# Kernel tuning notes

Hardware: AMD Instinct MI355X
Metric: run time of the kernel (lower is better)

Reference implementation:

```python
import jax, jax.numpy as jnp
import numpy as np

B, L, K, D = 1024, 128, 16, 512
NUM_FEATURES, NUM_LABELS, NUM_NEG = 100000, 131072, 2048
EPS = 0.1
C = 2.0 + EPS  # spherical kernel constant


def safe_log(x, eps=1e-08):
    return jnp.log(jnp.maximum(x, eps))


def safe_normalize(x, axis=-1, eps=0.0001):
    norm = jnp.linalg.norm(x, axis=axis, keepdims=True)
    return x / jnp.maximum(norm, eps)


def setup_inputs() -> dict:
    key = jax.random.key(0)
    k0, k1, k2, k3, k4 = jax.random.split(key, 5)
    indices = jax.random.randint(k0, (B, L), 0, NUM_FEATURES)
    mask = jnp.ones((B, L), jnp.float32)
    labels = jax.random.randint(k1, (B, K), 0, NUM_LABELS)
    label_mask = jnp.ones((B, K), jnp.float32)
    neg_indices = jax.random.randint(k2, (NUM_NEG,), 0, NUM_LABELS)
    embed_table = jax.random.normal(k3, (NUM_FEATURES, D), jnp.float32) * 0.02
    W_kernel = jax.random.normal(k4, (D, NUM_LABELS), jnp.float32) * 0.02  # nnx.Linear kernel (in, out)
    return {"indices": indices, "mask": mask, "labels": labels,
            "label_mask": label_mask, "neg_indices": neg_indices,
            "embed_table": embed_table, "W_kernel": W_kernel}


def reference(indices, mask, labels, label_mask, neg_indices, embed_table, W_kernel):
    # MeanEmbedding encoder
    embeds = embed_table[indices]                                  # [B, L, D]
    sum_embeds = jnp.sum(embeds * mask[:, :, None], axis=1)        # [B, D]
    enc = sum_embeds / jnp.maximum(jnp.sum(mask, axis=1, keepdims=True), 1.0)
    query = safe_normalize(enc, axis=-1)                           # [B, D]
    W = safe_normalize(W_kernel.T, axis=-1)                        # [NUM_LABELS, D]

    safe_labels = jnp.maximum(labels, 0)
    all_indices = jnp.concatenate([safe_labels.reshape(-1), neg_indices])  # [B*K + NN]
    W_subset = W[all_indices]                                      # [B*K+NN, D]

    # spherical Yat kernel: dot^2 / max(C - 2*dot, eps)
    dot = jnp.clip(query @ W_subset.T, -0.999, 0.999)              # [B, B*K+NN]
    scores = dot ** 2 / jnp.maximum(C - 2.0 * dot, EPS)

    idx_offsets = jnp.arange(B)[:, None] * K + jnp.arange(K)[None, :]
    pos_scores = jnp.take_along_axis(scores, idx_offsets, axis=1)  # [B, K]
    neg_scores = scores[:, B * K:]                                 # [B, NN]
    all_scores = jnp.concatenate([pos_scores, neg_scores], axis=1) + 1e-08
    log_Z = jax.scipy.special.logsumexp(safe_log(all_scores), axis=1)
    log_probs = safe_log(pos_scores + 1e-08) - log_Z[:, None]
    return -jnp.sum(log_probs * label_mask) / (jnp.sum(label_mask) + 1e-06)
```

## Files before the change

### kernel.cpp

```cpp
#include <hip/hip_runtime.h>
#include <hip/hip_bf16.h>

#define BDIM 1024
#define LDIM 128
#define KDIM 16
#define DDIM 512
#define NFEAT 100000
#define NLAB 131072
#define NNEG 2048
#define NPOS (BDIM * KDIM)
#define NSUB (NPOS + NNEG)
#define EPSV 0.1f
#define CV 2.1f

typedef __attribute__((ext_vector_type(8))) short s8v;
typedef __attribute__((ext_vector_type(4))) float f4v;

static __device__ __forceinline__ unsigned short f2bf(float x) {
    union { float f; unsigned u; } v; v.f = x;
    unsigned r = v.u + 0x7FFF + ((v.u >> 16) & 1);
    return (unsigned short)(r >> 16);
}
static __device__ __forceinline__ float bf2f(unsigned short h) {
    return __uint_as_float((unsigned)h << 16);
}

__global__ __launch_bounds__(256) void init_kernel(int* __restrict__ cnt,
                                                   float* __restrict__ norms2,
                                                   float* __restrict__ Zrow,
                                                   float* __restrict__ accum) {
    int j = blockIdx.x * 256 + threadIdx.x;
    cnt[j] = 0;
    if (j < NSUB) norms2[j] = 0.f;
    if (j < BDIM) Zrow[j] = 0.f;
    if (j < 2) accum[j] = 0.f;
}

__global__ __launch_bounds__(256) void count_kernel(const int* __restrict__ labels,
                                                    const int* __restrict__ negs,
                                                    int* __restrict__ all_idx,
                                                    int* __restrict__ cnt) {
    int j = blockIdx.x * 256 + threadIdx.x;
    if (j >= NSUB) return;
    int v = (j < NPOS) ? max(labels[j], 0) : negs[j - NPOS];
    all_idx[j] = v;
    atomicAdd(&cnt[v], 1);
}

__global__ __launch_bounds__(256) void scan1_kernel(const int* __restrict__ cnt,
                                                    int* __restrict__ offs,
                                                    int* __restrict__ bsum) {
    int t = threadIdx.x;
    int base = blockIdx.x * 512;
    int a0 = cnt[base + 2 * t], a1 = cnt[base + 2 * t + 1];
    int chunk = a0 + a1;
    int ts = chunk;
    int lane = t & 63, wid = t >> 6;
    #pragma unroll
    for (int off = 1; off < 64; off <<= 1) {
        int v = __shfl_up(ts, off, 64);
        if (lane >= off) ts += v;
    }
    __shared__ int wsum[4];
    if (lane == 63) wsum[wid] = ts;
    __syncthreads();
    int woff = 0;
    for (int w = 0; w < wid; ++w) woff += wsum[w];
    int incl = woff + ts;
    int excl = incl - chunk;
    offs[base + 2 * t]     = excl;
    offs[base + 2 * t + 1] = excl + a0;
    if (t == 255) bsum[blockIdx.x] = incl;
}

__global__ __launch_bounds__(256) void scan2_kernel(const int* __restrict__ bsum,
                                                    int* __restrict__ bofs) {
    int t = threadIdx.x;
    int a = bsum[t];
    int ts = a;
    int lane = t & 63, wid = t >> 6;
    #pragma unroll
    for (int off = 1; off < 64; off <<= 1) {
        int v = __shfl_up(ts, off, 64);
        if (lane >= off) ts += v;
    }
    __shared__ int wsum[4];
    if (lane == 63) wsum[wid] = ts;
    __syncthreads();
    int woff = 0;
    for (int w = 0; w < wid; ++w) woff += wsum[w];
    bofs[t] = woff + ts - a;
}

__global__ __launch_bounds__(256) void scan3_kernel(int* __restrict__ offs,
                                                    const int* __restrict__ bofs) {
    int v = blockIdx.x * 256 + threadIdx.x;
    offs[v] += bofs[v >> 9];
}

__global__ __launch_bounds__(256) void place_kernel(const int* __restrict__ all_idx,
                                                    int* __restrict__ offs,
                                                    int* __restrict__ srt_v,
                                                    int* __restrict__ rank) {
    int j = blockIdx.x * 256 + threadIdx.x;
    if (j >= NSUB) return;
    int v = all_idx[j];
    int r = atomicAdd(&offs[v], 1);
    srt_v[r] = v;
    rank[j] = r;
}

__global__ __launch_bounds__(256) void query_kernel(const int* __restrict__ indices,
                                                    const float* __restrict__ mask,
                                                    const float* __restrict__ embed,
                                                    float* __restrict__ query,
                                                    unsigned short* __restrict__ qbf) {
    __shared__ int   sidx[LDIM];
    __shared__ float smask[LDIM];
    int b = blockIdx.x;
    int t = threadIdx.x;
    if (t < LDIM) {
        sidx[t]  = indices[b * LDIM + t];
        smask[t] = mask[b * LDIM + t];
    }
    __syncthreads();

    float ax = 0.f, ay = 0.f, msum = 0.f;
    #pragma unroll 2
    for (int l = 0; l < LDIM; l += 4) {
        int   i0 = sidx[l],     i1 = sidx[l + 1],  i2 = sidx[l + 2],  i3 = sidx[l + 3];
        float m0 = smask[l],    m1 = smask[l + 1], m2 = smask[l + 2], m3 = smask[l + 3];
        float2 r0 = *(const float2*)&embed[(size_t)i0 * DDIM + t * 2];
        float2 r1 = *(const float2*)&embed[(size_t)i1 * DDIM + t * 2];
        float2 r2 = *(const float2*)&embed[(size_t)i2 * DDIM + t * 2];
        float2 r3 = *(const float2*)&embed[(size_t)i3 * DDIM + t * 2];
        msum += m0 + m1 + m2 + m3;
        ax += m0 * r0.x + m1 * r1.x + m2 * r2.x + m3 * r3.x;
        ay += m0 * r0.y + m1 * r1.y + m2 * r2.y + m3 * r3.y;
    }
    float denom = fmaxf(msum, 1.0f);
    ax /= denom; ay /= denom;

    float ss = ax * ax + ay * ay;
    #pragma unroll
    for (int off = 32; off > 0; off >>= 1) ss += __shfl_down(ss, off, 64);
    __shared__ float red[4];
    __shared__ float snorm;
    int wid = t >> 6, lane = t & 63;
    if (lane == 0) red[wid] = ss;
    __syncthreads();
    if (t == 0) snorm = sqrtf(red[0] + red[1] + red[2] + red[3]);
    __syncthreads();
    float inv = 1.f / fmaxf(snorm, 1e-4f);
    float2 o = { ax * inv, ay * inv };
    *(float2*)&query[(size_t)b * DDIM + t * 2] = o;
    ushort2 ob = { f2bf(o.x), f2bf(o.y) };
    *(ushort2*)&qbf[(size_t)b * DDIM + t * 2] = ob;
}

__global__ __launch_bounds__(256) void gather_kernel(const float* __restrict__ Wk,
                                                     const int* __restrict__ srt_v,
                                                     unsigned short* __restrict__ Wsrt) {
    int d = blockIdx.x;
    int half = blockIdx.y;
    const float* row = Wk + (size_t)d * NLAB;
    unsigned short* o = Wsrt + (size_t)d * NSUB;
    int r0 = half * (NSUB / 2), r1 = r0 + NSUB / 2;
    #pragma unroll 4
    for (int r = r0 + threadIdx.x; r < r1; r += 256) {
        int v = srt_v[r];
        o[r] = f2bf(__builtin_nontemporal_load(&row[v]));
    }
}

__global__ __launch_bounds__(256) void transpose_kernel(const unsigned short* __restrict__ Wsrt,
                                                        unsigned short* __restrict__ WT,
                                                        float* __restrict__ norms2) {
    __shared__ unsigned short tile[64][66];
    __shared__ float psum[64];
    int t = threadIdx.x;
    int r0 = blockIdx.x * 64;
    int d0 = blockIdx.y * 64;
    if (t < 64) psum[t] = 0.f;
    __syncthreads();
    float local = 0.f;
    int rl = t & 63;
    #pragma unroll 4
    for (int it = 0; it < 16; ++it) {
        int dl = it * 4 + (t >> 6);
        unsigned short v = Wsrt[(size_t)(d0 + dl) * NSUB + r0 + rl];
        tile[rl][dl] = v;
        float f = bf2f(v);
        local += f * f;
    }
    atomicAdd(&psum[rl], local);
    __syncthreads();
    #pragma unroll 4
    for (int it = 0; it < 16; ++it) {
        int rr = it * 4 + (t >> 6);
        WT[(size_t)(r0 + rr) * DDIM + d0 + rl] = tile[rr][rl];
    }
    if (t < 64) atomicAdd(&norms2[r0 + t], psum[t]);
}

__global__ __launch_bounds__(256) void pos_kernel(const float* __restrict__ query,
                                                  const unsigned short* __restrict__ WT,
                                                  const int* __restrict__ rank,
                                                  const float* __restrict__ norms2,
                                                  float* __restrict__ pos_scores,
                                                  float* __restrict__ Zrow) {
    int t = threadIdx.x;
    int w = t >> 6, l = t & 63;
    int b = blockIdx.x * 4 + w;
    int j = b * KDIM + (l & 15);
    int r = rank[j];
    int g = l >> 4;
    const unsigned short* wrow = WT + (size_t)r * DDIM + g * 128;
    const float* qrow = query + (size_t)b * DDIM + g * 128;
    float acc = 0.f;
    #pragma unroll
    for (int kk = 0; kk < 128; kk += 8) {
        ushort4 w0 = *(const ushort4*)&wrow[kk];
        ushort4 w1 = *(const ushort4*)&wrow[kk + 4];
        float4 q0 = *(const float4*)&qrow[kk];
        float4 q1 = *(const float4*)&qrow[kk + 4];
        acc += bf2f(w0.x) * q0.x + bf2f(w0.y) * q0.y + bf2f(w0.z) * q0.z + bf2f(w0.w) * q0.w
             + bf2f(w1.x) * q1.x + bf2f(w1.y) * q1.y + bf2f(w1.z) * q1.z + bf2f(w1.w) * q1.w;
    }
    acc += __shfl_xor(acc, 16, 64);
    acc += __shfl_xor(acc, 32, 64);
    if (l < 16) {
        float nrm = fmaxf(sqrtf(norms2[r]), 1e-4f);
        float dot = fminf(fmaxf(acc / nrm, -0.999f), 0.999f);
        float sc = dot * dot / fmaxf(CV - 2.f * dot, EPSV);
        pos_scores[j] = sc;
        float s = sc;
        s += __shfl_xor(s, 1, 64); s += __shfl_xor(s, 2, 64);
        s += __shfl_xor(s, 4, 64); s += __shfl_xor(s, 8, 64);
        if (l == 0) atomicAdd(&Zrow[b], s);
    }
}

static __device__ __forceinline__ float score_of(float acc, float nn) {
    float dot = acc / nn;
    dot = fminf(fmaxf(dot, -0.999f), 0.999f);
    return dot * dot / fmaxf(CV - 2.f * dot, EPSV);
}

__global__ __launch_bounds__(256) void neg_kernel(const unsigned short* __restrict__ qbf,
                                                  const unsigned short* __restrict__ WT,
                                                  const int* __restrict__ rank,
                                                  const float* __restrict__ norms2,
                                                  float* __restrict__ Zrow) {
    __shared__ float rowsum[64];
    int t = threadIdx.x;
    int w = t >> 6, l = t & 63;
    int wm = w >> 1, wn = w & 1;
    int lr = l & 15, lg = l >> 4;
    int m0 = blockIdx.x * 64 + wm * 32;
    int n0 = blockIdx.y * 64 + wn * 32;
    if (t < 64) rowsum[t] = 0.f;
    __syncthreads();

    int rB0 = rank[NPOS + n0 + lr];
    int rB1 = rank[NPOS + n0 + 16 + lr];
    const unsigned short* a0p = qbf + (size_t)(m0 + lr) * DDIM + lg * 8;
    const unsigned short* a1p = qbf + (size_t)(m0 + 16 + lr) * DDIM + lg * 8;
    const unsigned short* b0p = WT + (size_t)rB0 * DDIM + lg * 8;
    const unsigned short* b1p = WT + (size_t)rB1 * DDIM + lg * 8;

    f4v acc00 = {0.f, 0.f, 0.f, 0.f}, acc01 = acc00, acc10 = acc00, acc11 = acc00;
    #pragma unroll
    for (int k0 = 0; k0 < DDIM; k0 += 32) {
        s8v a0 = *(const s8v*)(a0p + k0);
        s8v a1 = *(const s8v*)(a1p + k0);
        s8v b0 = *(const s8v*)(b0p + k0);
        s8v b1 = *(const s8v*)(b1p + k0);
        acc00 = __builtin_amdgcn_mfma_f32_16x16x32_bf16(a0, b0, acc00, 0, 0, 0);
        acc01 = __builtin_amdgcn_mfma_f32_16x16x32_bf16(a0, b1, acc01, 0, 0, 0);
        acc10 = __builtin_amdgcn_mfma_f32_16x16x32_bf16(a1, b0, acc10, 0, 0, 0);
        acc11 = __builtin_amdgcn_mfma_f32_16x16x32_bf16(a1, b1, acc11, 0, 0, 0);
    }

    float nn0 = fmaxf(sqrtf(norms2[rB0]), 1e-4f);
    float nn1 = fmaxf(sqrtf(norms2[rB1]), 1e-4f);
    float s[8];
    #pragma unroll
    for (int i = 0; i < 4; ++i) {
        s[i]     = score_of(acc00[i], nn0) + score_of(acc01[i], nn1);
        s[4 + i] = score_of(acc10[i], nn0) + score_of(acc11[i], nn1);
    }
    #pragma unroll
    for (int i = 0; i < 8; ++i) {
        s[i] += __shfl_xor(s[i], 1, 64);
        s[i] += __shfl_xor(s[i], 2, 64);
        s[i] += __shfl_xor(s[i], 4, 64);
        s[i] += __shfl_xor(s[i], 8, 64);
    }
    if (lr == 0) {
        #pragma unroll
        for (int i = 0; i < 4; ++i) {
            atomicAdd(&rowsum[wm * 32 + lg * 4 + i], s[i]);
            atomicAdd(&rowsum[wm * 32 + 16 + lg * 4 + i], s[4 + i]);
        }
    }
    __syncthreads();
    if (t < 64) atomicAdd(&Zrow[blockIdx.x * 64 + t], rowsum[t]);
}

__global__ __launch_bounds__(256) void finalize_kernel(const float* __restrict__ pos_scores,
                                                       const float* __restrict__ label_mask,
                                                       const float* __restrict__ Zrow,
                                                       float* __restrict__ accum) {
    int j = blockIdx.x * 256 + threadIdx.x;
    int b = j >> 4;
    float lm = label_mask[j];
    float logZ = logf(Zrow[b] + (float)(KDIM + NNEG) * 1e-8f);
    float v = lm * (logf(pos_scores[j] + 1e-8f) - logZ);
    #pragma unroll
    for (int off = 32; off > 0; off >>= 1) {
        v  += __shfl_down(v, off, 64);
        lm += __shfl_down(lm, off, 64);
    }
    __shared__ float rv[4], rl[4];
    int wid = threadIdx.x >> 6, lane = threadIdx.x & 63;
    if (lane == 0) { rv[wid] = v; rl[wid] = lm; }
    __syncthreads();
    if (threadIdx.x == 0) {
        atomicAdd(&accum[0], rv[0] + rv[1] + rv[2] + rv[3]);
        atomicAdd(&accum[1], rl[0] + rl[1] + rl[2] + rl[3]);
    }
}

__global__ void writeout_kernel(const float* __restrict__ accum, float* __restrict__ out) {
    out[0] = -accum[0] / (accum[1] + 1e-6f);
}

extern "C" void kernel_launch(void* const* d_in, const int* in_sizes, int n_in,
                              void* d_out, int out_size, void* d_ws, size_t ws_size,
                              hipStream_t stream) {
    const int*   indices    = (const int*)  d_in[0];
    const float* mask       = (const float*)d_in[1];
    const int*   labels     = (const int*)  d_in[2];
    const float* label_mask = (const float*)d_in[3];
    const int*   negs       = (const int*)  d_in[4];
    const float* embed      = (const float*)d_in[5];
    const float* Wk         = (const float*)d_in[6];
    float* out = (float*)d_out;

    unsigned short* Wsrt = (unsigned short*)d_ws;
    unsigned short* WT   = Wsrt + (size_t)DDIM * NSUB;
    float* query      = (float*)(WT + (size_t)NSUB * DDIM);
    unsigned short* qbf = (unsigned short*)(query + (size_t)BDIM * DDIM);
    int*   all_idx    = (int*)(qbf + (size_t)BDIM * DDIM);
    int*   srt_v      = all_idx + NSUB;
    int*   rank       = srt_v + NSUB;
    float* norms2     = (float*)(rank + NSUB);
    float* pos_scores = norms2 + NSUB;
    float* Zrow       = pos_scores + NPOS;
    float* accum      = Zrow + BDIM;
    int*   cnt        = (int*)(accum + 2);
    int*   offs       = cnt + NLAB;
    int*   bsum       = offs + NLAB;
    int*   bofs       = bsum + 256;

    init_kernel<<<NLAB / 256, 256, 0, stream>>>(cnt, norms2, Zrow, accum);
    count_kernel<<<NSUB / 256, 256, 0, stream>>>(labels, negs, all_idx, cnt);
    query_kernel<<<BDIM, 256, 0, stream>>>(indices, mask, embed, query, qbf);
    scan1_kernel<<<NLAB / 512, 256, 0, stream>>>(cnt, offs, bsum);
    scan2_kernel<<<1, 256, 0, stream>>>(bsum, bofs);
    scan3_kernel<<<NLAB / 256, 256, 0, stream>>>(offs, bofs);
    place_kernel<<<NSUB / 256, 256, 0, stream>>>(all_idx, offs, srt_v, rank);
    gather_kernel<<<dim3(DDIM, 2), 256, 0, stream>>>(Wk, srt_v, Wsrt);
    transpose_kernel<<<dim3(NSUB / 64, DDIM / 64), 256, 0, stream>>>(Wsrt, WT, norms2);
    pos_kernel<<<NPOS / 64, 256, 0, stream>>>(query, WT, rank, norms2, pos_scores, Zrow);
    neg_kernel<<<dim3(BDIM / 64, NNEG / 64), 256, 0, stream>>>(qbf, WT, rank, norms2, Zrow);
    finalize_kernel<<<NPOS / 256, 256, 0, stream>>>(pos_scores, label_mask, Zrow, accum);
    writeout_kernel<<<1, 1, 0, stream>>>(accum, out);
}
```

Before: 152.5 us.

## Coarsen label sort buckets, fuse gather with transpose, merge kernels and drop writeout

Label sorting now uses 512 coarse buckets keyed on the high bits of the index instead of a full 131072-entry counting sort. That removes the large init and the three-pass scan in favour of a single one-block scan. The W gather is fused into the transpose, so columns are read straight from W_kernel into the shared tile, and the intermediate Wsrt buffer plus one kernel launch go away. The query and gather-transpose kernels are merged into one launch, as are the pos and neg scoring kernels. The final writeout moves into finalize through a last-block ticket. This cuts launch count and intermediate memory traffic, but the gather reads within a 64-row tile are now strided and less coalesced.

```diff
diff --git a/kernel.cpp b/kernel.cpp
--- a/kernel.cpp
+++ b/kernel.cpp
@@ -5,13 +5,14 @@
 #define LDIM 128
 #define KDIM 16
 #define DDIM 512
-#define NFEAT 100000
 #define NLAB 131072
 #define NNEG 2048
 #define NPOS (BDIM * KDIM)
 #define NSUB (NPOS + NNEG)
 #define EPSV 0.1f
 #define CV 2.1f
+#define NBUCK 512
+#define GT_BLOCKS ((NSUB / 64) * (DDIM / 64))
 
 typedef __attribute__((ext_vector_type(8))) short s8v;
 typedef __attribute__((ext_vector_type(4))) float f4v;
@@ -28,12 +29,14 @@
 __global__ __launch_bounds__(256) void init_kernel(int* __restrict__ cnt,
                                                    float* __restrict__ norms2,
                                                    float* __restrict__ Zrow,
-                                                   float* __restrict__ accum) {
+                                                   float* __restrict__ accum,
+                                                   int* __restrict__ ticket) {
     int j = blockIdx.x * 256 + threadIdx.x;
-    cnt[j] = 0;
     if (j < NSUB) norms2[j] = 0.f;
+    if (j < NBUCK) cnt[j] = 0;
     if (j < BDIM) Zrow[j] = 0.f;
     if (j < 2) accum[j] = 0.f;
+    if (j == 0) *ticket = 0;
 }
 
 __global__ __launch_bounds__(256) void count_kernel(const int* __restrict__ labels,
@@ -44,15 +47,13 @@
     if (j >= NSUB) return;
     int v = (j < NPOS) ? max(labels[j], 0) : negs[j - NPOS];
     all_idx[j] = v;
-    atomicAdd(&cnt[v], 1);
-}
-
-__global__ __launch_bounds__(256) void scan1_kernel(const int* __restrict__ cnt,
-                                                    int* __restrict__ offs,
-                                                    int* __restrict__ bsum) {
+    atomicAdd(&cnt[v >> 8], 1);
+}
+
+__global__ __launch_bounds__(256) void scan_kernel(const int* __restrict__ cnt,
+                                                   int* __restrict__ offs) {
     int t = threadIdx.x;
-    int base = blockIdx.x * 512;
-    int a0 = cnt[base + 2 * t], a1 = cnt[base + 2 * t + 1];
+    int a0 = cnt[2 * t], a1 = cnt[2 * t + 1];
     int chunk = a0 + a1;
     int ts = chunk;
     int lane = t & 63, wid = t >> 6;
@@ -68,34 +69,8 @@
     for (int w = 0; w < wid; ++w) woff += wsum[w];
     int incl = woff + ts;
     int excl = incl - chunk;
-    offs[base + 2 * t]     = excl;
-    offs[base + 2 * t + 1] = excl + a0;
-    if (t == 255) bsum[blockIdx.x] = incl;
-}
-
-__global__ __launch_bounds__(256) void scan2_kernel(const int* __restrict__ bsum,
-                                                    int* __restrict__ bofs) {
-    int t = threadIdx.x;
-    int a = bsum[t];
-    int ts = a;
-    int lane = t & 63, wid = t >> 6;
-    #pragma unroll
-    for (int off = 1; off < 64; off <<= 1) {
-        int v = __shfl_up(ts, off, 64);
-        if (lane >= off) ts += v;
-    }
-    __shared__ int wsum[4];
-    if (lane == 63) wsum[wid] = ts;
-    __syncthreads();
-    int woff = 0;
-    for (int w = 0; w < wid; ++w) woff += wsum[w];
-    bofs[t] = woff + ts - a;
-}
-
-__global__ __launch_bounds__(256) void scan3_kernel(int* __restrict__ offs,
-                                                    const int* __restrict__ bofs) {
-    int v = blockIdx.x * 256 + threadIdx.x;
-    offs[v] += bofs[v >> 9];
+    offs[2 * t]     = excl;
+    offs[2 * t + 1] = excl + a0;
 }
 
 __global__ __launch_bounds__(256) void place_kernel(const int* __restrict__ all_idx,
@@ -105,139 +80,89 @@
     int j = blockIdx.x * 256 + threadIdx.x;
     if (j >= NSUB) return;
     int v = all_idx[j];
-    int r = atomicAdd(&offs[v], 1);
+    int r = atomicAdd(&offs[v >> 8], 1);
     srt_v[r] = v;
     rank[j] = r;
 }
 
-__global__ __launch_bounds__(256) void query_kernel(const int* __restrict__ indices,
+__global__ __launch_bounds__(256) void main1_kernel(const float* __restrict__ Wk,
+                                                    const int* __restrict__ srt_v,
+                                                    unsigned short* __restrict__ WT,
+                                                    float* __restrict__ norms2,
+                                                    const int* __restrict__ indices,
                                                     const float* __restrict__ mask,
                                                     const float* __restrict__ embed,
                                                     float* __restrict__ query,
                                                     unsigned short* __restrict__ qbf) {
-    __shared__ int   sidx[LDIM];
-    __shared__ float smask[LDIM];
-    int b = blockIdx.x;
     int t = threadIdx.x;
-    if (t < LDIM) {
-        sidx[t]  = indices[b * LDIM + t];
-        smask[t] = mask[b * LDIM + t];
-    }
-    __syncthreads();
-
-    float ax = 0.f, ay = 0.f, msum = 0.f;
-    #pragma unroll 2
-    for (int l = 0; l < LDIM; l += 4) {
-        int   i0 = sidx[l],     i1 = sidx[l + 1],  i2 = sidx[l + 2],  i3 = sidx[l + 3];
-        float m0 = smask[l],    m1 = smask[l + 1], m2 = smask[l + 2], m3 = smask[l + 3];
-        float2 r0 = *(const float2*)&embed[(size_t)i0 * DDIM + t * 2];
-        float2 r1 = *(const float2*)&embed[(size_t)i1 * DDIM + t * 2];
-        float2 r2 = *(const float2*)&embed[(size_t)i2 * DDIM + t * 2];
-        float2 r3 = *(const float2*)&embed[(size_t)i3 * DDIM + t * 2];
-        msum += m0 + m1 + m2 + m3;
-        ax += m0 * r0.x + m1 * r1.x + m2 * r2.x + m3 * r3.x;
-        ay += m0 * r0.y + m1 * r1.y + m2 * r2.y + m3 * r3.y;
-    }
-    float denom = fmaxf(msum, 1.0f);
-    ax /= denom; ay /= denom;
-
-    float ss = ax * ax + ay * ay;
-    #pragma unroll
-    for (int off = 32; off > 0; off >>= 1) ss += __shfl_down(ss, off, 64);
-    __shared__ float red[4];
-    __shared__ float snorm;
-    int wid = t >> 6, lane = t & 63;
-    if (lane == 0) red[wid] = ss;
-    __syncthreads();
-    if (t == 0) snorm = sqrtf(red[0] + red[1] + red[2] + red[3]);
-    __syncthreads();
-    float inv = 1.f / fmaxf(snorm, 1e-4f);
-    float2 o = { ax * inv, ay * inv };
-    *(float2*)&query[(size_t)b * DDIM + t * 2] = o;
-    ushort2 ob = { f2bf(o.x), f2bf(o.y) };
-    *(ushort2*)&qbf[(size_t)b * DDIM + t * 2] = ob;
-}
-
-__global__ __launch_bounds__(256) void gather_kernel(const float* __restrict__ Wk,
-                                                     const int* __restrict__ srt_v,
-                                                     unsigned short* __restrict__ Wsrt) {
-    int d = blockIdx.x;
-    int half = blockIdx.y;
-    const float* row = Wk + (size_t)d * NLAB;
-    unsigned short* o = Wsrt + (size_t)d * NSUB;
-    int r0 = half * (NSUB / 2), r1 = r0 + NSUB / 2;
-    #pragma unroll 4
-    for (int r = r0 + threadIdx.x; r < r1; r += 256) {
-        int v = srt_v[r];
-        o[r] = f2bf(__builtin_nontemporal_load(&row[v]));
-    }
-}
-
-__global__ __launch_bounds__(256) void transpose_kernel(const unsigned short* __restrict__ Wsrt,
-                                                        unsigned short* __restrict__ WT,
-                                                        float* __restrict__ norms2) {
-    __shared__ unsigned short tile[64][66];
-    __shared__ float psum[64];
-    int t = threadIdx.x;
-    int r0 = blockIdx.x * 64;
-    int d0 = blockIdx.y * 64;
-    if (t < 64) psum[t] = 0.f;
-    __syncthreads();
-    float local = 0.f;
-    int rl = t & 63;
-    #pragma unroll 4
-    for (int it = 0; it < 16; ++it) {
-        int dl = it * 4 + (t >> 6);
-        unsigned short v = Wsrt[(size_t)(d0 + dl) * NSUB + r0 + rl];
-        tile[rl][dl] = v;
-        float f = bf2f(v);
-        local += f * f;
-    }
-    atomicAdd(&psum[rl], local);
-    __syncthreads();
-    #pragma unroll 4
-    for (int it = 0; it < 16; ++it) {
-        int rr = it * 4 + (t >> 6);
-        WT[(size_t)(r0 + rr) * DDIM + d0 + rl] = tile[rr][rl];
-    }
-    if (t < 64) atomicAdd(&norms2[r0 + t], psum[t]);
-}
-
-__global__ __launch_bounds__(256) void pos_kernel(const float* __restrict__ query,
-                                                  const unsigned short* __restrict__ WT,
-                                                  const int* __restrict__ rank,
-                                                  const float* __restrict__ norms2,
-                                                  float* __restrict__ pos_scores,
-                                                  float* __restrict__ Zrow) {
-    int t = threadIdx.x;
-    int w = t >> 6, l = t & 63;
-    int b = blockIdx.x * 4 + w;
-    int j = b * KDIM + (l & 15);
-    int r = rank[j];
-    int g = l >> 4;
-    const unsigned short* wrow = WT + (size_t)r * DDIM + g * 128;
-    const float* qrow = query + (size_t)b * DDIM + g * 128;
-    float acc = 0.f;
-    #pragma unroll
-    for (int kk = 0; kk < 128; kk += 8) {
-        ushort4 w0 = *(const ushort4*)&wrow[kk];
-        ushort4 w1 = *(const ushort4*)&wrow[kk + 4];
-        float4 q0 = *(const float4*)&qrow[kk];
-        float4 q1 = *(const float4*)&qrow[kk + 4];
-        acc += bf2f(w0.x) * q0.x + bf2f(w0.y) * q0.y + bf2f(w0.z) * q0.z + bf2f(w0.w) * q0.w
-             + bf2f(w1.x) * q1.x + bf2f(w1.y) * q1.y + bf2f(w1.z) * q1.z + bf2f(w1.w) * q1.w;
-    }
-    acc += __shfl_xor(acc, 16, 64);
-    acc += __shfl_xor(acc, 32, 64);
-    if (l < 16) {
-        float nrm = fmaxf(sqrtf(norms2[r]), 1e-4f);
-        float dot = fminf(fmaxf(acc / nrm, -0.999f), 0.999f);
-        float sc = dot * dot / fmaxf(CV - 2.f * dot, EPSV);
-        pos_scores[j] = sc;
-        float s = sc;
-        s += __shfl_xor(s, 1, 64); s += __shfl_xor(s, 2, 64);
-        s += __shfl_xor(s, 4, 64); s += __shfl_xor(s, 8, 64);
-        if (l == 0) atomicAdd(&Zrow[b], s);
+    if (blockIdx.x < GT_BLOCKS) {
+        __shared__ unsigned short tile[64][66];
+        __shared__ float psum[64];
+        int bt = blockIdx.x;
+        int rt = bt % (NSUB / 64);
+        int dt = bt / (NSUB / 64);
+        int r0 = rt * 64, d0 = dt * 64;
+        int l = t & 63, w = t >> 6;
+        if (t < 64) psum[t] = 0.f;
+        __syncthreads();
+        int v = srt_v[r0 + l];
+        float local = 0.f;
+        #pragma unroll
+        for (int i = 0; i < 16; ++i) {
+            int dl = w * 16 + i;
+            float f = __builtin_nontemporal_load(&Wk[(size_t)(d0 + dl) * NLAB + v]);
+            unsigned short h = f2bf(f);
+            tile[l][dl] = h;
+            float bf = bf2f(h);
+            local += bf * bf;
+        }
+        atomicAdd(&psum[l], local);
+        __syncthreads();
+        #pragma unroll
+        for (int i = 0; i < 16; ++i) {
+            int rr = w * 16 + i;
+            WT[(size_t)(r0 + rr) * DDIM + d0 + l] = tile[rr][l];
+        }
+        if (t < 64) atomicAdd(&norms2[r0 + t], psum[t]);
+    } else {
+        __shared__ int   sidx[LDIM];
+        __shared__ float smask[LDIM];
+        __shared__ float red[4];
+        __shared__ float snorm;
+        int b = blockIdx.x - GT_BLOCKS;
+        if (t < LDIM) {
+            sidx[t]  = indices[b * LDIM + t];
+            smask[t] = mask[b * LDIM + t];
+        }
+        __syncthreads();
+        float ax = 0.f, ay = 0.f, msum = 0.f;
+        #pragma unroll 2
+        for (int l = 0; l < LDIM; l += 4) {
+            int   i0 = sidx[l],   i1 = sidx[l + 1],  i2 = sidx[l + 2],  i3 = sidx[l + 3];
+            float m0 = smask[l],  m1 = smask[l + 1], m2 = smask[l + 2], m3 = smask[l + 3];
+            float2 r0 = *(const float2*)&embed[(size_t)i0 * DDIM + t * 2];
+            float2 r1 = *(const float2*)&embed[(size_t)i1 * DDIM + t * 2];
+            float2 r2 = *(const float2*)&embed[(size_t)i2 * DDIM + t * 2];
+            float2 r3 = *(const float2*)&embed[(size_t)i3 * DDIM + t * 2];
+            msum += m0 + m1 + m2 + m3;
+            ax += m0 * r0.x + m1 * r1.x + m2 * r2.x + m3 * r3.x;
+            ay += m0 * r0.y + m1 * r1.y + m2 * r2.y + m3 * r3.y;
+        }
+        float denom = fmaxf(msum, 1.0f);
+        ax /= denom; ay /= denom;
+        float ss = ax * ax + ay * ay;
+        #pragma unroll
+        for (int off = 32; off > 0; off >>= 1) ss += __shfl_down(ss, off, 64);
+        int wid = t >> 6, lane = t & 63;
+        if (lane == 0) red[wid] = ss;
+        __syncthreads();
+        if (t == 0) snorm = sqrtf(red[0] + red[1] + red[2] + red[3]);
+        __syncthreads();
+        float inv = 1.f / fmaxf(snorm, 1e-4f);
+        float2 o = { ax * inv, ay * inv };
+        *(float2*)&query[(size_t)b * DDIM + t * 2] = o;
+        ushort2 ob = { f2bf(o.x), f2bf(o.y) };
+        *(ushort2*)&qbf[(size_t)b * DDIM + t * 2] = ob;
     }
 }
 
@@ -247,71 +172,109 @@
     return dot * dot / fmaxf(CV - 2.f * dot, EPSV);
 }
 
-__global__ __launch_bounds__(256) void neg_kernel(const unsigned short* __restrict__ qbf,
-                                                  const unsigned short* __restrict__ WT,
-                                                  const int* __restrict__ rank,
-                                                  const float* __restrict__ norms2,
-                                                  float* __restrict__ Zrow) {
-    __shared__ float rowsum[64];
+__global__ __launch_bounds__(256) void main2_kernel(const unsigned short* __restrict__ qbf,
+                                                    const float* __restrict__ query,
+                                                    const unsigned short* __restrict__ WT,
+                                                    const int* __restrict__ rank,
+                                                    const float* __restrict__ norms2,
+                                                    float* __restrict__ pos_scores,
+                                                    float* __restrict__ Zrow) {
     int t = threadIdx.x;
     int w = t >> 6, l = t & 63;
-    int wm = w >> 1, wn = w & 1;
-    int lr = l & 15, lg = l >> 4;
-    int m0 = blockIdx.x * 64 + wm * 32;
-    int n0 = blockIdx.y * 64 + wn * 32;
-    if (t < 64) rowsum[t] = 0.f;
-    __syncthreads();
-
-    int rB0 = rank[NPOS + n0 + lr];
-    int rB1 = rank[NPOS + n0 + 16 + lr];
-    const unsigned short* a0p = qbf + (size_t)(m0 + lr) * DDIM + lg * 8;
-    const unsigned short* a1p = qbf + (size_t)(m0 + 16 + lr) * DDIM + lg * 8;
-    const unsigned short* b0p = WT + (size_t)rB0 * DDIM + lg * 8;
-    const unsigned short* b1p = WT + (size_t)rB1 * DDIM + lg * 8;
-
-    f4v acc00 = {0.f, 0.f, 0.f, 0.f}, acc01 = acc00, acc10 = acc00, acc11 = acc00;
-    #pragma unroll
-    for (int k0 = 0; k0 < DDIM; k0 += 32) {
-        s8v a0 = *(const s8v*)(a0p + k0);
-        s8v a1 = *(const s8v*)(a1p + k0);
-        s8v b0 = *(const s8v*)(b0p + k0);
-        s8v b1 = *(const s8v*)(b1p + k0);
-        acc00 = __builtin_amdgcn_mfma_f32_16x16x32_bf16(a0, b0, acc00, 0, 0, 0);
-        acc01 = __builtin_amdgcn_mfma_f32_16x16x32_bf16(a0, b1, acc01, 0, 0, 0);
-        acc10 = __builtin_amdgcn_mfma_f32_16x16x32_bf16(a1, b0, acc10, 0, 0, 0);
-        acc11 = __builtin_amdgcn_mfma_f32_16x16x32_bf16(a1, b1, acc11, 0, 0, 0);
-    }
-
-    float nn0 = fmaxf(sqrtf(norms2[rB0]), 1e-4f);
-    float nn1 = fmaxf(sqrtf(norms2[rB1]), 1e-4f);
-    float s[8];
-    #pragma unroll
-    for (int i = 0; i < 4; ++i) {
-        s[i]     = score_of(acc00[i], nn0) + score_of(acc01[i], nn1);
-        s[4 + i] = score_of(acc10[i], nn0) + score_of(acc11[i], nn1);
-    }
-    #pragma unroll
-    for (int i = 0; i < 8; ++i) {
-        s[i] += __shfl_xor(s[i], 1, 64);
-        s[i] += __shfl_xor(s[i], 2, 64);
-        s[i] += __shfl_xor(s[i], 4, 64);
-        s[i] += __shfl_xor(s[i], 8, 64);
-    }
-    if (lr == 0) {
+    if (blockIdx.x < (BDIM / 64) * (NNEG / 64)) {
+        __shared__ float rowsum[64];
+        int bx = blockIdx.x;
+        int mt = bx & 15, nt = bx >> 4;
+        int wm = w >> 1, wn = w & 1;
+        int lr = l & 15, lg = l >> 4;
+        int m0 = mt * 64 + wm * 32;
+        int n0 = nt * 64 + wn * 32;
+        if (t < 64) rowsum[t] = 0.f;
+        __syncthreads();
+
+        int rB0 = rank[NPOS + n0 + lr];
+        int rB1 = rank[NPOS + n0 + 16 + lr];
+        const unsigned short* a0p = qbf + (size_t)(m0 + lr) * DDIM + lg * 8;
+        const unsigned short* a1p = qbf + (size_t)(m0 + 16 + lr) * DDIM + lg * 8;
+        const unsigned short* b0p = WT + (size_t)rB0 * DDIM + lg * 8;
+        const unsigned short* b1p = WT + (size_t)rB1 * DDIM + lg * 8;
+
+        f4v acc00 = {0.f, 0.f, 0.f, 0.f}, acc01 = acc00, acc10 = acc00, acc11 = acc00;
+        #pragma unroll
+        for (int k0 = 0; k0 < DDIM; k0 += 32) {
+            s8v a0 = *(const s8v*)(a0p + k0);
+            s8v a1 = *(const s8v*)(a1p + k0);
+            s8v b0 = *(const s8v*)(b0p + k0);
+            s8v b1 = *(const s8v*)(b1p + k0);
+            acc00 = __builtin_amdgcn_mfma_f32_16x16x32_bf16(a0, b0, acc00, 0, 0, 0);
+            acc01 = __builtin_amdgcn_mfma_f32_16x16x32_bf16(a0, b1, acc01, 0, 0, 0);
+            acc10 = __builtin_amdgcn_mfma_f32_16x16x32_bf16(a1, b0, acc10, 0, 0, 0);
+            acc11 = __builtin_amdgcn_mfma_f32_16x16x32_bf16(a1, b1, acc11, 0, 0, 0);
+        }
+
+        float nn0 = fmaxf(sqrtf(norms2[rB0]), 1e-4f);
+        float nn1 = fmaxf(sqrtf(norms2[rB1]), 1e-4f);
+        float s[8];
         #pragma unroll
         for (int i = 0; i < 4; ++i) {
-            atomicAdd(&rowsum[wm * 32 + lg * 4 + i], s[i]);
-            atomicAdd(&rowsum[wm * 32 + 16 + lg * 4 + i], s[4 + i]);
-        }
-    }
-    __syncthreads();
-    if (t < 64) atomicAdd(&Zrow[blockIdx.x * 64 + t], rowsum[t]);
+            s[i]     = score_of(acc00[i], nn0) + score_of(acc01[i], nn1);
+            s[4 + i] = score_of(acc10[i], nn0) + score_of(acc11[i], nn1);
+        }
+        #pragma unroll
+        for (int i = 0; i < 8; ++i) {
+            s[i] += __shfl_xor(s[i], 1, 64);
+            s[i] += __shfl_xor(s[i], 2, 64);
+            s[i] += __shfl_xor(s[i], 4, 64);
+            s[i] += __shfl_xor(s[i], 8, 64);
+        }
+        if (lr == 0) {
+            #pragma unroll
+            for (int i = 0; i < 4; ++i) {
+                atomicAdd(&rowsum[wm * 32 + lg * 4 + i], s[i]);
+                atomicAdd(&rowsum[wm * 32 + 16 + lg * 4 + i], s[4 + i]);
+            }
+        }
+        __syncthreads();
+        if (t < 64) atomicAdd(&Zrow[mt * 64 + t], rowsum[t]);
+    } else {
+        int px = blockIdx.x - (BDIM / 64) * (NNEG / 64);
+        int b = px * 4 + w;
+        int j = b * KDIM + (l & 15);
+        int r = rank[j];
+        int g = l >> 4;
+        const unsigned short* wrow = WT + (size_t)r * DDIM + g * 128;
+        const float* qrow = query + (size_t)b * DDIM + g * 128;
+        float acc = 0.f;
+        #pragma unroll
+        for (int kk = 0; kk < 128; kk += 8) {
+            ushort4 w0 = *(const ushort4*)&wrow[kk];
+            ushort4 w1 = *(const ushort4*)&wrow[kk + 4];
+            float4 q0 = *(const float4*)&qrow[kk];
+            float4 q1 = *(const float4*)&qrow[kk + 4];
+            acc += bf2f(w0.x) * q0.x + bf2f(w0.y) * q0.y + bf2f(w0.z) * q0.z + bf2f(w0.w) * q0.w
+                 + bf2f(w1.x) * q1.x + bf2f(w1.y) * q1.y + bf2f(w1.z) * q1.z + bf2f(w1.w) * q1.w;
+        }
+        acc += __shfl_xor(acc, 16, 64);
+        acc += __shfl_xor(acc, 32, 64);
+        if (l < 16) {
+            float nrm = fmaxf(sqrtf(norms2[r]), 1e-4f);
+            float dot = fminf(fmaxf(acc / nrm, -0.999f), 0.999f);
+            float sc = dot * dot / fmaxf(CV - 2.f * dot, EPSV);
+            pos_scores[j] = sc;
+            float s = sc;
+            s += __shfl_xor(s, 1, 64); s += __shfl_xor(s, 2, 64);
+            s += __shfl_xor(s, 4, 64); s += __shfl_xor(s, 8, 64);
+            if (l == 0) atomicAdd(&Zrow[b], s);
+        }
+    }
 }
 
 __global__ __launch_bounds__(256) void finalize_kernel(const float* __restrict__ pos_scores,
                                                        const float* __restrict__ label_mask,
                                                        const float* __restrict__ Zrow,
-                                                       float* __restrict__ accum) {
+                                                       float* __restrict__ accum,
+                                                       int* __restrict__ ticket,
+                                                       float* __restrict__ out) {
     int j = blockIdx.x * 256 + threadIdx.x;
     int b = j >> 4;
     float lm = label_mask[j];
@@ -329,11 +292,14 @@
     if (threadIdx.x == 0) {
         atomicAdd(&accum[0], rv[0] + rv[1] + rv[2] + rv[3]);
         atomicAdd(&accum[1], rl[0] + rl[1] + rl[2] + rl[3]);
-    }
-}
-
-__global__ void writeout_kernel(const float* __restrict__ accum, float* __restrict__ out) {
-    out[0] = -accum[0] / (accum[1] + 1e-6f);
+        __threadfence();
+        int old = atomicAdd(ticket, 1);
+        if (old == (int)gridDim.x - 1) {
+            float a = atomicAdd(&accum[0], 0.f);
+            float m = atomicAdd(&accum[1], 0.f);
+            out[0] = -a / (m + 1e-6f);
+        }
+    }
 }
 
 extern "C" void kernel_launch(void* const* d_in, const int* in_sizes, int n_in,
@@ -348,8 +314,7 @@
     const float* Wk         = (const float*)d_in[6];
     float* out = (float*)d_out;
 
-    unsigned short* Wsrt = (unsigned short*)d_ws;
-    unsigned short* WT   = Wsrt + (size_t)DDIM * NSUB;
+    unsigned short* WT  = (unsigned short*)d_ws;
     float* query      = (float*)(WT + (size_t)NSUB * DDIM);
     unsigned short* qbf = (unsigned short*)(query + (size_t)BDIM * DDIM);
     int*   all_idx    = (int*)(qbf + (size_t)BDIM * DDIM);
@@ -359,22 +324,18 @@
     float* pos_scores = norms2 + NSUB;
     float* Zrow       = pos_scores + NPOS;
     float* accum      = Zrow + BDIM;
-    int*   cnt        = (int*)(accum + 2);
-    int*   offs       = cnt + NLAB;
-    int*   bsum       = offs + NLAB;
-    int*   bofs       = bsum + 256;
-
-    init_kernel<<<NLAB / 256, 256, 0, stream>>>(cnt, norms2, Zrow, accum);
+    int*   ticket     = (int*)(accum + 2);
+    int*   cnt        = ticket + 1;
+    int*   offs       = cnt + NBUCK;
+
+    init_kernel<<<NSUB / 256, 256, 0, stream>>>(cnt, norms2, Zrow, accum, ticket);
     count_kernel<<<NSUB / 256, 256, 0, stream>>>(labels, negs, all_idx, cnt);
-    query_kernel<<<BDIM, 256, 0, stream>>>(indices, mask, embed, query, qbf);
-    scan1_kernel<<<NLAB / 512, 256, 0, stream>>>(cnt, offs, bsum);
-    scan2_kernel<<<1, 256, 0, stream>>>(bsum, bofs);
-    scan3_kernel<<<NLAB / 256, 256, 0, stream>>>(offs, bofs);
+    scan_kernel<<<1, 256, 0, stream>>>(cnt, offs);
     place_kernel<<<NSUB / 256, 256, 0, stream>>>(all_idx, offs, srt_v, rank);
-    gather_kernel<<<dim3(DDIM, 2), 256, 0, stream>>>(Wk, srt_v, Wsrt);
-    transpose_kernel<<<dim3(NSUB / 64, DDIM / 64), 256, 0, stream>>>(Wsrt, WT, norms2);
-    pos_kernel<<<NPOS / 64, 256, 0, stream>>>(query, WT, rank, norms2, pos_scores, Zrow);
-    neg_kernel<<<dim3(BDIM / 64, NNEG / 64), 256, 0, stream>>>(qbf, WT, rank, norms2, Zrow);
-    finalize_kernel<<<NPOS / 256, 256, 0, stream>>>(pos_scores, label_mask, Zrow, accum);
-    writeout_kernel<<<1, 1, 0, stream>>>(accum, out);
-}
+    main1_kernel<<<GT_BLOCKS + BDIM, 256, 0, stream>>>(Wk, srt_v, WT, norms2,
+                                                       indices, mask, embed, query, qbf);
+    main2_kernel<<<(BDIM / 64) * (NNEG / 64) + NPOS / 64, 256, 0, stream>>>(
+        qbf, query, WT, rank, norms2, pos_scores, Zrow);
+    finalize_kernel<<<NPOS / 256, 256, 0, stream>>>(pos_scores, label_mask, Zrow,
+                                                    accum, ticket, out);
+}
```

Result: no change. 152.1 us (-0.2%).
